# Optimization experiments

Measured on AMD Instinct MI355X. Metric: run time of the kernel, lower is better.

## Reference

```python
import jax, jax.numpy as jnp
import numpy as np

NUM_CLASSES = 10000
FEATURE_DIMS = 2048
BATCH = 512


def setup_inputs() -> dict:
    key = jax.random.key(0)
    k1, k2, k3 = jax.random.split(key, 3)
    features = jax.random.normal(k1, (BATCH, FEATURE_DIMS), dtype=jnp.float32)
    centers = jax.random.normal(k2, (NUM_CLASSES, FEATURE_DIMS), dtype=jnp.float32)
    targets = jax.random.randint(k3, (BATCH,), 0, NUM_CLASSES, dtype=jnp.int64)
    return {"features": features, "centers": centers, "targets": targets}


def reference(features, centers, targets):
    # dist_mat[i, j] = ||f_i||^2 + ||c_j||^2 - 2 f_i . c_j   -> [B, C]
    f_sq = jnp.sum(features * features, axis=1, keepdims=True)       # [B, 1]
    c_sq = jnp.sum(centers * centers, axis=1)[None, :]               # [1, C]
    dist_mat = f_sq + c_sq - 2.0 * jnp.einsum('bd,cd->bc', features, centers)
    # gather the true-class distance per sample (the original does this via a
    # boolean-mask loop; each row's mask selects exactly one entry)
    tgt = targets.astype(jnp.int32)
    dist = jnp.take_along_axis(dist_mat, tgt[:, None], axis=1)[:, 0]  # [B]
    dist = jnp.clip(dist, 1e-12, 1e12)
    return jnp.mean(dist)
```

## Files before the change

kernel.cpp:

```cpp
#include <hip/hip_runtime.h>

#define BATCH 512
#define DIMS  2048

__global__ __launch_bounds__(256) void center_dist_kernel(
        const float* __restrict__ features,
        const float* __restrict__ centers,
        const int* __restrict__ targets,
        float* __restrict__ dists) {
    const int b = blockIdx.x;
    const int t = targets[b];
    const float4* f = reinterpret_cast<const float4*>(features + (size_t)b * DIMS);
    const float4* c = reinterpret_cast<const float4*>(centers + (size_t)t * DIMS);

    float acc = 0.f;
    #pragma unroll 2
    for (int i = threadIdx.x; i < DIMS / 4; i += 256) {
        float4 fv = f[i];
        float4 cv = c[i];
        float dx = fv.x - cv.x;
        float dy = fv.y - cv.y;
        float dz = fv.z - cv.z;
        float dw = fv.w - cv.w;
        acc += dx * dx + dy * dy + dz * dz + dw * dw;
    }

    #pragma unroll
    for (int off = 32; off > 0; off >>= 1) acc += __shfl_down(acc, off, 64);

    __shared__ float s[4];
    const int lane = threadIdx.x & 63;
    const int wid  = threadIdx.x >> 6;
    if (lane == 0) s[wid] = acc;
    __syncthreads();
    if (threadIdx.x == 0) {
        float d = s[0] + s[1] + s[2] + s[3];
        d = fminf(fmaxf(d, 1e-12f), 1e12f);
        dists[b] = d;
    }
}

__global__ __launch_bounds__(256) void mean_kernel(
        const float* __restrict__ dists,
        float* __restrict__ out) {
    float acc = 0.f;
    #pragma unroll 2
    for (int i = threadIdx.x; i < BATCH; i += 256) acc += dists[i];

    #pragma unroll
    for (int off = 32; off > 0; off >>= 1) acc += __shfl_down(acc, off, 64);

    __shared__ float s[4];
    const int lane = threadIdx.x & 63;
    const int wid  = threadIdx.x >> 6;
    if (lane == 0) s[wid] = acc;
    __syncthreads();
    if (threadIdx.x == 0) out[0] = (s[0] + s[1] + s[2] + s[3]) * (1.0f / BATCH);
}

extern "C" void kernel_launch(void* const* d_in, const int* in_sizes, int n_in,
                              void* d_out, int out_size, void* d_ws, size_t ws_size,
                              hipStream_t stream) {
    const float* features = (const float*)d_in[0];
    const float* centers  = (const float*)d_in[1];
    const int*   targets  = (const int*)d_in[2];
    float* out   = (float*)d_out;
    float* dists = (float*)d_ws;

    center_dist_kernel<<<BATCH, 256, 0, stream>>>(features, centers, targets, dists);
    mean_kernel<<<1, 256, 0, stream>>>(dists, out);
}
```

Baseline: 11.55 us.

## Fuse distance and mean kernels via last-block atomic counter

Merges the per-sample distance kernel and the mean-reduction kernel into one launch. Each block publishes its distance and increments a global counter, and the last block performs the final mean. This removes the second kernel launch but adds a memset to reset the counter, plus atomic release/acquire traffic per block.

```diff
diff --git a/kernel.cpp b/kernel.cpp
--- a/kernel.cpp
+++ b/kernel.cpp
@@ -3,11 +3,14 @@
 #define BATCH 512
 #define DIMS  2048
 
-__global__ __launch_bounds__(256) void center_dist_kernel(
+__global__ __launch_bounds__(256) void center_loss_fused(
         const float* __restrict__ features,
         const float* __restrict__ centers,
         const int* __restrict__ targets,
-        float* __restrict__ dists) {
+        float* __restrict__ out,
+        float* __restrict__ ws_d,
+        unsigned* __restrict__ counter)
+{
     const int b = blockIdx.x;
     const int t = targets[b];
     const float4* f = reinterpret_cast<const float4*>(features + (size_t)b * DIMS);
@@ -29,33 +32,35 @@
     for (int off = 32; off > 0; off >>= 1) acc += __shfl_down(acc, off, 64);
 
     __shared__ float s[4];
+    __shared__ bool is_last;
     const int lane = threadIdx.x & 63;
     const int wid  = threadIdx.x >> 6;
     if (lane == 0) s[wid] = acc;
     __syncthreads();
+
     if (threadIdx.x == 0) {
         float d = s[0] + s[1] + s[2] + s[3];
         d = fminf(fmaxf(d, 1e-12f), 1e12f);
-        dists[b] = d;
+        __hip_atomic_store(&ws_d[b], d, __ATOMIC_RELEASE, __HIP_MEMORY_SCOPE_AGENT);
+        unsigned old = __hip_atomic_fetch_add(counter, 1u, __ATOMIC_ACQ_REL,
+                                              __HIP_MEMORY_SCOPE_AGENT);
+        is_last = (old == BATCH - 1);
     }
-}
+    __syncthreads();
 
-__global__ __launch_bounds__(256) void mean_kernel(
-        const float* __restrict__ dists,
-        float* __restrict__ out) {
-    float acc = 0.f;
-    #pragma unroll 2
-    for (int i = threadIdx.x; i < BATCH; i += 256) acc += dists[i];
-
-    #pragma unroll
-    for (int off = 32; off > 0; off >>= 1) acc += __shfl_down(acc, off, 64);
-
-    __shared__ float s[4];
-    const int lane = threadIdx.x & 63;
-    const int wid  = threadIdx.x >> 6;
-    if (lane == 0) s[wid] = acc;
-    __syncthreads();
-    if (threadIdx.x == 0) out[0] = (s[0] + s[1] + s[2] + s[3]) * (1.0f / BATCH);
+    if (is_last) {
+        float a2 = 0.f;
+        #pragma unroll 2
+        for (int i = threadIdx.x; i < BATCH; i += 256)
+            a2 += __hip_atomic_load(&ws_d[i], __ATOMIC_ACQUIRE,
+                                    __HIP_MEMORY_SCOPE_AGENT);
+        #pragma unroll
+        for (int off = 32; off > 0; off >>= 1) a2 += __shfl_down(a2, off, 64);
+        if (lane == 0) s[wid] = a2;
+        __syncthreads();
+        if (threadIdx.x == 0)
+            out[0] = (s[0] + s[1] + s[2] + s[3]) * (1.0f / BATCH);
+    }
 }
 
 extern "C" void kernel_launch(void* const* d_in, const int* in_sizes, int n_in,
@@ -64,9 +69,12 @@
     const float* features = (const float*)d_in[0];
     const float* centers  = (const float*)d_in[1];
     const int*   targets  = (const int*)d_in[2];
-    float* out   = (float*)d_out;
-    float* dists = (float*)d_ws;
+    float* out = (float*)d_out;
 
-    center_dist_kernel<<<BATCH, 256, 0, stream>>>(features, centers, targets, dists);
-    mean_kernel<<<1, 256, 0, stream>>>(dists, out);
+    float*    ws_d    = (float*)d_ws;
+    unsigned* counter = (unsigned*)((char*)d_ws + BATCH * sizeof(float));
+
+    hipMemsetAsync(counter, 0, sizeof(unsigned), stream);
+    center_loss_fused<<<BATCH, 256, 0, stream>>>(features, centers, targets,
+                                                 out, ws_d, counter);
 }
```

Result: slower. 24.86 us (+115.3%).
